# Kernel tuning notes

Hardware: AMD Instinct MI355X
Metric: run time of the kernel (lower is better)

## Reference

```python
import jax, jax.numpy as jnp
import numpy as np

N_NODES = 100000
N_EDGES = 1600000
D = 128        # in_dim == hidden_dim (forced by x_j + xe in message)
C = 64         # num_classes
G = 128        # number of graphs in the batch
BN_EPS = 1e-5


def setup_inputs() -> dict:
    key = jax.random.key(0)
    ks = jax.random.split(key, 14)
    s = 0.05
    inp = {
        "x": jax.random.normal(ks[0], (N_NODES, D), dtype=jnp.float32),
        "xe": jax.random.normal(ks[1], (N_EDGES, D), dtype=jnp.float32),
        "edge_index": jax.random.randint(ks[2], (2, N_EDGES), 0, N_NODES, dtype=jnp.int32),
        "batch": jnp.sort(jax.random.randint(ks[3], (N_NODES,), 0, G, dtype=jnp.int32)),
        # layer 0 MySAGEConv params
        "Wl0": jax.random.normal(ks[4], (D, D), dtype=jnp.float32) * s,
        "bl0": jnp.zeros((D,), dtype=jnp.float32),
        "Wr0": jax.random.normal(ks[5], (D, D), dtype=jnp.float32) * s,
        # layer 1 MySAGEConv params
        "Wl1": jax.random.normal(ks[6], (D, D), dtype=jnp.float32) * s,
        "bl1": jnp.zeros((D,), dtype=jnp.float32),
        "Wr1": jax.random.normal(ks[7], (D, D), dtype=jnp.float32) * s,
        # BatchNorm (only applied after non-final layers -> layer 0)
        "gamma0": jnp.ones((D,), dtype=jnp.float32),
        "beta0": jnp.zeros((D,), dtype=jnp.float32),
        # readout projection
        "Wp": jax.random.normal(ks[8], (C, D), dtype=jnp.float32) * s,
        "bp": jnp.zeros((C,), dtype=jnp.float32),
    }
    return inp


def _segment_mean(vals, idx, num_segments):
    s = jax.ops.segment_sum(vals, idx, num_segments=num_segments)
    cnt = jax.ops.segment_sum(jnp.ones((vals.shape[0],), vals.dtype), idx,
                              num_segments=num_segments)
    return s / jnp.clip(cnt, 1.0)[:, None]


def _my_sage_conv(h, xe, src, dst, Wl, bl, Wr):
    # message: relu(x_j + xe); aggregate: scatter-mean at dst; then lin_l + lin_r
    msg = jax.nn.relu(h[src] + xe)                       # [E, D]
    agg = _segment_mean(msg, dst, N_NODES)               # [N, D]
    return agg @ Wl.T + bl + h @ Wr.T


def _batchnorm_train(h, gamma, beta):
    mu = jnp.mean(h, axis=0)
    var = jnp.var(h, axis=0)
    return gamma * (h - mu) * jax.lax.rsqrt(var + BN_EPS) + beta


def reference(x, xe, edge_index, batch,
              Wl0, bl0, Wr0, Wl1, bl1, Wr1,
              gamma0, beta0, Wp, bp):
    src, dst = edge_index[0], edge_index[1]
    # layer 0: conv -> BN -> ReLU
    h = _my_sage_conv(x, xe, src, dst, Wl0, bl0, Wr0)
    h = jax.nn.relu(_batchnorm_train(h, gamma0, beta0))
    # layer 1 (last): conv only
    h = _my_sage_conv(h, xe, src, dst, Wl1, bl1, Wr1)
    # graph readout (global mean pool over pre-proj node features)
    g = _segment_mean(h, batch, G)                       # [G, D]
    # readout projection on nodes
    h = jax.nn.relu(h) @ Wp.T + bp                       # [N, C]
    return h, g
```

## Files before the change

### kernel.cpp

```cpp
#include <hip/hip_runtime.h>

#define N_NODES 100000
#define N_EDGES 1600000
#define DIM 128
#define NCLS 64
#define NG 128
#define BN_EPS 1e-5f

typedef __attribute__((ext_vector_type(8))) short s16x8;
typedef __attribute__((ext_vector_type(4))) float f32x4;
#define MFMA_BF16 __builtin_amdgcn_mfma_f32_16x16x32_bf16

__device__ __forceinline__ unsigned short f2b(float x) {
    unsigned u = __float_as_uint(x);
    return (unsigned short)((u + 0x7FFFu + ((u >> 16) & 1u)) >> 16);
}
__device__ __forceinline__ float b2f(unsigned short s) {
    return __uint_as_float(((unsigned)s) << 16);
}
__device__ __forceinline__ float4 bexp4(ushort4 u) {
    float4 f;
    f.x = b2f(u.x); f.y = b2f(u.y); f.z = b2f(u.z); f.w = b2f(u.w);
    return f;
}

__device__ __forceinline__ void f2hl8(float4 v0, float4 v1, s16x8& h8, s16x8& l8) {
    float vv[8] = {v0.x, v0.y, v0.z, v0.w, v1.x, v1.y, v1.z, v1.w};
#pragma unroll
    for (int i = 0; i < 8; ++i) {
        unsigned u = __float_as_uint(vv[i]);
        short h = (short)(u >> 16);
        float r = vv[i] - __uint_as_float(u & 0xFFFF0000u);
        short l = (short)(__float_as_uint(r) >> 16);
        h8[i] = h;
        l8[i] = l;
    }
}

__global__ __launch_bounds__(256) void k_mega0(
        const float* __restrict__ Wl0, const float* __restrict__ Wr0,
        const float* __restrict__ Wl1, const float* __restrict__ Wr1,
        const float* __restrict__ Wp,
        short* __restrict__ fWl0h, short* __restrict__ fWl0l,
        short* __restrict__ fWr0h, short* __restrict__ fWr0l,
        short* __restrict__ fWl1h, short* __restrict__ fWl1l,
        short* __restrict__ fWr1h, short* __restrict__ fWr1l,
        short* __restrict__ fWph, short* __restrict__ fWpl,
        const float* __restrict__ x, unsigned short* __restrict__ x_bf,
        const int* __restrict__ dst, int* __restrict__ cnt) {
    int b = blockIdx.x;
    if (b < 36) {
        const float* W; short* hi; short* lo; int ct;
        if (b < 8)       { W = Wl0; hi = fWl0h; lo = fWl0l; ct = b; }
        else if (b < 16) { W = Wr0; hi = fWr0h; lo = fWr0l; ct = b - 8; }
        else if (b < 24) { W = Wl1; hi = fWl1h; lo = fWl1l; ct = b - 16; }
        else if (b < 32) { W = Wr1; hi = fWr1h; lo = fWr1l; ct = b - 24; }
        else             { W = Wp;  hi = fWph;  lo = fWpl;  ct = b - 32; }
        if (b >= 32 && ct >= 4) return;
        int tt = threadIdx.x;
        int lane = tt & 63, ks = (tt >> 6) & 3;
        int row = ct * 16 + (lane & 15);
        int k0 = ks * 32 + ((lane >> 4) << 3);
        float4 v0 = *reinterpret_cast<const float4*>(&W[(size_t)row * DIM + k0]);
        float4 v1 = *reinterpret_cast<const float4*>(&W[(size_t)row * DIM + k0 + 4]);
        s16x8 h8, l8;
        f2hl8(v0, v1, h8, l8);
        int t = ct * 256 + ks * 64 + lane;
        *reinterpret_cast<s16x8*>(&hi[(size_t)t * 8]) = h8;
        *reinterpret_cast<s16x8*>(&lo[(size_t)t * 8]) = l8;
    } else if (b < 36 + 6250) {
        int i = (b - 36) * 256 + threadIdx.x;
        float4 a = reinterpret_cast<const float4*>(x)[(size_t)i * 2];
        float4 c = reinterpret_cast<const float4*>(x)[(size_t)i * 2 + 1];
        ushort4 oa, ob;
        oa.x = f2b(a.x); oa.y = f2b(a.y); oa.z = f2b(a.z); oa.w = f2b(a.w);
        ob.x = f2b(c.x); ob.y = f2b(c.y); ob.z = f2b(c.z); ob.w = f2b(c.w);
        reinterpret_cast<ushort4*>(x_bf)[(size_t)i * 2] = oa;
        reinterpret_cast<ushort4*>(x_bf)[(size_t)i * 2 + 1] = ob;
    } else {
        int e = (b - 36 - 6250) * 256 + threadIdx.x;
        atomicAdd(&cnt[dst[e]], 1);
    }
}

__global__ void k_scan1(const int* __restrict__ cnt, int* __restrict__ rowptr,
                        int* __restrict__ bsums) {
    __shared__ int sd[1024];
    int tid = threadIdx.x;
    int i = blockIdx.x * 1024 + tid;
    int v = (i < N_NODES) ? cnt[i] : 0;
    sd[tid] = v;
    __syncthreads();
    for (int off = 1; off < 1024; off <<= 1) {
        int t2 = (tid >= off) ? sd[tid - off] : 0;
        __syncthreads();
        sd[tid] += t2;
        __syncthreads();
    }
    if (i < N_NODES) rowptr[i] = sd[tid] - v;
    if (tid == 1023) bsums[blockIdx.x] = sd[tid];
}

__global__ void k_scan2(int* __restrict__ bsums, int nb) {
    __shared__ int sd[128];
    int t = threadIdx.x;
    int v = (t < nb) ? bsums[t] : 0;
    sd[t] = v;
    __syncthreads();
    for (int off = 1; off < 128; off <<= 1) {
        int u = (t >= off) ? sd[t - off] : 0;
        __syncthreads();
        sd[t] += u;
        __syncthreads();
    }
    if (t < nb) bsums[t] = sd[t] - v;
}

__global__ void k_scan3(int* __restrict__ rowptr, const int* __restrict__ bsums,
                        int* __restrict__ wcur) {
    int i = blockIdx.x * 1024 + threadIdx.x;
    if (i < N_NODES) {
        int v = rowptr[i] + bsums[blockIdx.x];
        rowptr[i] = v;
        wcur[i] = v;
    }
    if (i == N_NODES - 1) rowptr[N_NODES] = N_EDGES;
}

__global__ void k_scatter(const int* __restrict__ src, const int* __restrict__ dst,
                          int* __restrict__ wcur, int2* __restrict__ esort) {
    int e = blockIdx.x * 256 + threadIdx.x;
    if (e < N_EDGES) {
        int d = dst[e];
        int p = atomicAdd(&wcur[d], 1);
        esort[p] = make_int2(e, src[e]);
    }
}

template <int MODE>
__global__ __launch_bounds__(256) void k_agg(
        const unsigned short* __restrict__ Fb, const float* __restrict__ xe,
        unsigned short* __restrict__ xe_s,
        const int* __restrict__ rowptr, const int2* __restrict__ esort,
        unsigned short* __restrict__ agg, const float* __restrict__ bnsc) {
    int wid = (blockIdx.x * 256 + threadIdx.x) >> 6;
    int lane = threadIdx.x & 63;
    if (wid >= N_NODES) return;
    int half = lane >> 5;
    int l = lane & 31;
    int p0 = rowptr[wid], p1 = rowptr[wid + 1];
    if (p0 == p1) {
        if (half == 0) {
            ushort4 z = make_ushort4(0, 0, 0, 0);
            *reinterpret_cast<ushort4*>(&agg[(size_t)wid * DIM + l * 4]) = z;
        }
        return;
    }
    float4 sc, sh;
    if (MODE != 0) {
        sc = *reinterpret_cast<const float4*>(&bnsc[l * 4]);
        sh = *reinterpret_cast<const float4*>(&bnsc[DIM + l * 4]);
    }
    float4 acc = make_float4(0.f, 0.f, 0.f, 0.f);
    for (int p = p0; p < p1; p += 8) {
#pragma unroll
        for (int j = 0; j < 4; ++j) {
            int q = p + j * 2 + half;
            int qc = min(q, p1 - 1);
            int2 es = esort[qc];
            float4 a = bexp4(*reinterpret_cast<const ushort4*>(
                &Fb[(size_t)es.y * DIM + l * 4]));
            float4 b;
            if (MODE == 1) {
                b = bexp4(*reinterpret_cast<const ushort4*>(
                    &xe_s[(size_t)qc * DIM + l * 4]));
            } else {
                b = *reinterpret_cast<const float4*>(
                    &xe[(size_t)es.x * DIM + l * 4]);
            }
            if (MODE != 0) {
                a.x = fmaxf(a.x * sc.x + sh.x, 0.f);
                a.y = fmaxf(a.y * sc.y + sh.y, 0.f);
                a.z = fmaxf(a.z * sc.z + sh.z, 0.f);
                a.w = fmaxf(a.w * sc.w + sh.w, 0.f);
            }
            if (q < p1) {
                if (MODE == 0) {
                    ushort4 o;
                    o.x = f2b(b.x); o.y = f2b(b.y);
                    o.z = f2b(b.z); o.w = f2b(b.w);
                    *reinterpret_cast<ushort4*>(&xe_s[(size_t)qc * DIM + l * 4]) = o;
                }
                acc.x += fmaxf(a.x + b.x, 0.f);
                acc.y += fmaxf(a.y + b.y, 0.f);
                acc.z += fmaxf(a.z + b.z, 0.f);
                acc.w += fmaxf(a.w + b.w, 0.f);
            }
        }
    }
    acc.x += __shfl_xor(acc.x, 32);
    acc.y += __shfl_xor(acc.y, 32);
    acc.z += __shfl_xor(acc.z, 32);
    acc.w += __shfl_xor(acc.w, 32);
    if (half == 0) {
        float s = 1.f / (float)(p1 - p0);
        ushort4 o;
        o.x = f2b(acc.x * s); o.y = f2b(acc.y * s);
        o.z = f2b(acc.z * s); o.w = f2b(acc.w * s);
        *reinterpret_cast<ushort4*>(&agg[(size_t)wid * DIM + l * 4]) = o;
    }
}

__global__ __launch_bounds__(256) void k_gemm2(
        const unsigned short* __restrict__ Abf, const unsigned short* __restrict__ Bbf,
        const short* __restrict__ fW1h, const short* __restrict__ fW1l,
        const short* __restrict__ fW2h, const short* __restrict__ fW2l,
        const float* __restrict__ bias, unsigned short* __restrict__ OUTb,
        float* __restrict__ bnacc, const float* __restrict__ bnsc,
        int doBN, int bnB) {
    int t = threadIdx.x, w = t >> 6, l = t & 63;
    int n0 = blockIdx.x * 128;
    int r = l & 15, kh = l >> 4;
    int row0 = n0 + w * 16 + r;
    int row1 = row0 + 64;
    int n_0 = min(row0, N_NODES - 1);
    int n_1 = min(row1, N_NODES - 1);

    f32x4 acc0[8], acc1[8];
#pragma unroll
    for (int ct = 0; ct < 8; ++ct) {
        acc0[ct] = (f32x4){0.f, 0.f, 0.f, 0.f};
        acc1[ct] = (f32x4){0.f, 0.f, 0.f, 0.f};
    }
    const s16x8* w1h = (const s16x8*)fW1h;
    const s16x8* w1l = (const s16x8*)fW1l;
    const s16x8* w2h = (const s16x8*)fW2h;
    const s16x8* w2l = (const s16x8*)fW2l;

#pragma unroll
    for (int ks = 0; ks < 4; ++ks) {
        int kb = ks * 32 + kh * 8;
        s16x8 a0 = *reinterpret_cast<const s16x8*>(&Abf[(size_t)n_0 * DIM + kb]);
        s16x8 a1 = *reinterpret_cast<const s16x8*>(&Abf[(size_t)n_1 * DIM + kb]);
        s16x8 b0 = *reinterpret_cast<const s16x8*>(&Bbf[(size_t)n_0 * DIM + kb]);
        s16x8 b1 = *reinterpret_cast<const s16x8*>(&Bbf[(size_t)n_1 * DIM + kb]);
        if (bnB) {
            float4 sc0 = *reinterpret_cast<const float4*>(&bnsc[kb]);
            float4 sh0 = *reinterpret_cast<const float4*>(&bnsc[DIM + kb]);
            float4 sc1 = *reinterpret_cast<const float4*>(&bnsc[kb + 4]);
            float4 sh1 = *reinterpret_cast<const float4*>(&bnsc[DIM + kb + 4]);
            float scv[8] = {sc0.x, sc0.y, sc0.z, sc0.w, sc1.x, sc1.y, sc1.z, sc1.w};
            float shv[8] = {sh0.x, sh0.y, sh0.z, sh0.w, sh1.x, sh1.y, sh1.z, sh1.w};
#pragma unroll
            for (int i = 0; i < 8; ++i) {
                float v = b2f((unsigned short)b0[i]);
                b0[i] = (short)f2b(fmaxf(v * scv[i] + shv[i], 0.f));
                v = b2f((unsigned short)b1[i]);
                b1[i] = (short)f2b(fmaxf(v * scv[i] + shv[i], 0.f));
            }
        }
        int fb = ks * 64 + l;
#pragma unroll
        for (int ct = 0; ct < 8; ++ct) {
            int fi = ct * 256 + fb;
            s16x8 wh1 = w1h[fi], wl1 = w1l[fi];
            s16x8 wh2 = w2h[fi], wl2 = w2l[fi];
            acc0[ct] = MFMA_BF16(a0, wh1, acc0[ct], 0, 0, 0);
            acc0[ct] = MFMA_BF16(a0, wl1, acc0[ct], 0, 0, 0);
            acc0[ct] = MFMA_BF16(b0, wh2, acc0[ct], 0, 0, 0);
            acc0[ct] = MFMA_BF16(b0, wl2, acc0[ct], 0, 0, 0);
            acc1[ct] = MFMA_BF16(a1, wh1, acc1[ct], 0, 0, 0);
            acc1[ct] = MFMA_BF16(a1, wl1, acc1[ct], 0, 0, 0);
            acc1[ct] = MFMA_BF16(b1, wh2, acc1[ct], 0, 0, 0);
            acc1[ct] = MFMA_BF16(b1, wl2, acc1[ct], 0, 0, 0);
        }
    }

    float p1s[8], p2s[8];
    int col0 = l & 15;
    int nb0 = n0 + w * 16 + (kh << 2);
    int nb1 = nb0 + 64;
#pragma unroll
    for (int ct = 0; ct < 8; ++ct) {
        float bj = bias[ct * 16 + col0];
        float s1 = 0.f, s2 = 0.f;
#pragma unroll
        for (int rr = 0; rr < 4; ++rr) {
            int n = nb0 + rr;
            float h = acc0[ct][rr] + bj;
            if (n < N_NODES) {
                OUTb[(size_t)n * DIM + ct * 16 + col0] = f2b(h);
                s1 += h; s2 += h * h;
            }
            n = nb1 + rr;
            h = acc1[ct][rr] + bj;
            if (n < N_NODES) {
                OUTb[(size_t)n * DIM + ct * 16 + col0] = f2b(h);
                s1 += h; s2 += h * h;
            }
        }
        p1s[ct] = s1; p2s[ct] = s2;
    }
    if (doBN) {
        __shared__ float red1[512];
        __shared__ float red2[512];
#pragma unroll
        for (int ct = 0; ct < 8; ++ct) {
            p1s[ct] += __shfl_xor(p1s[ct], 16);
            p1s[ct] += __shfl_xor(p1s[ct], 32);
            p2s[ct] += __shfl_xor(p2s[ct], 16);
            p2s[ct] += __shfl_xor(p2s[ct], 32);
        }
        if (l < 16) {
#pragma unroll
            for (int ct = 0; ct < 8; ++ct) {
                red1[w * 128 + ct * 16 + l] = p1s[ct];
                red2[w * 128 + ct * 16 + l] = p2s[ct];
            }
        }
        __syncthreads();
        if (t < 128) {
            float s1 = red1[t] + red1[128 + t] + red1[256 + t] + red1[384 + t];
            float s2 = red2[t] + red2[128 + t] + red2[256 + t] + red2[384 + t];
            atomicAdd(&bnacc[t], s1);
            atomicAdd(&bnacc[128 + t], s2);
        }
    }
}

__global__ void k_bnfinal(const float* __restrict__ bnacc, const float* __restrict__ gamma,
                          const float* __restrict__ beta, float* __restrict__ bnsc) {
    int d = threadIdx.x;
    if (d < DIM) {
        float mu = bnacc[d] / (float)N_NODES;
        float var = bnacc[128 + d] / (float)N_NODES - mu * mu;
        float rstd = rsqrtf(var + BN_EPS);
        float sc = gamma[d] * rstd;
        bnsc[d] = sc;
        bnsc[128 + d] = beta[d] - mu * sc;
    }
}

__global__ void k_pool(const unsigned short* __restrict__ H1b,
                       const int* __restrict__ batch, float* __restrict__ gout) {
    __shared__ float red[4][128];
    int g = blockIdx.x;
    int t = threadIdx.x;
    int d = t & 127;
    int sl = t >> 7;
    int lo = 0, hi = N_NODES;
    while (lo < hi) { int m = (lo + hi) >> 1; if (batch[m] < g) lo = m + 1; else hi = m; }
    int s = lo;
    lo = 0; hi = N_NODES;
    while (lo < hi) { int m = (lo + hi) >> 1; if (batch[m] < g + 1) lo = m + 1; else hi = m; }
    int e = lo;
    float sum = 0.f;
    for (int n = s + sl; n < e; n += 4) sum += b2f(H1b[(size_t)n * DIM + d]);
    red[sl][d] = sum;
    __syncthreads();
    if (t < 128) {
        float tot = red[0][d] + red[1][d] + red[2][d] + red[3][d];
        gout[g * DIM + d] = tot / (float)max(e - s, 1);
    }
}

__global__ __launch_bounds__(256) void k_proj(
        const unsigned short* __restrict__ H1b, const short* __restrict__ fWph,
        const short* __restrict__ fWpl, const float* __restrict__ bp,
        float* __restrict__ OUT) {
    int t = threadIdx.x, w = t >> 6, l = t & 63;
    int n0 = blockIdx.x * 128;
    int r = l & 15, kh = l >> 4;
    int row0 = n0 + w * 16 + r;
    int row1 = row0 + 64;
    int n_0 = min(row0, N_NODES - 1);
    int n_1 = min(row1, N_NODES - 1);
    f32x4 acc0[4], acc1[4];
#pragma unroll
    for (int ct = 0; ct < 4; ++ct) {
        acc0[ct] = (f32x4){0.f, 0.f, 0.f, 0.f};
        acc1[ct] = (f32x4){0.f, 0.f, 0.f, 0.f};
    }
    const s16x8* wph = (const s16x8*)fWph;
    const s16x8* wpl = (const s16x8*)fWpl;
#pragma unroll
    for (int ks = 0; ks < 4; ++ks) {
        int kb = ks * 32 + kh * 8;
        s16x8 r0 = *reinterpret_cast<const s16x8*>(&H1b[(size_t)n_0 * DIM + kb]);
        s16x8 r1 = *reinterpret_cast<const s16x8*>(&H1b[(size_t)n_1 * DIM + kb]);
        s16x8 a0, a1;
#pragma unroll
        for (int i = 0; i < 8; ++i) {
            a0[i] = r0[i] < 0 ? (short)0 : r0[i];
            a1[i] = r1[i] < 0 ? (short)0 : r1[i];
        }
        int fb = ks * 64 + l;
#pragma unroll
        for (int ct = 0; ct < 4; ++ct) {
            int fi = ct * 256 + fb;
            s16x8 wh = wph[fi], wl = wpl[fi];
            acc0[ct] = MFMA_BF16(a0, wh, acc0[ct], 0, 0, 0);
            acc0[ct] = MFMA_BF16(a0, wl, acc0[ct], 0, 0, 0);
            acc1[ct] = MFMA_BF16(a1, wh, acc1[ct], 0, 0, 0);
            acc1[ct] = MFMA_BF16(a1, wl, acc1[ct], 0, 0, 0);
        }
    }
    int col0 = l & 15;
    int nb0 = n0 + w * 16 + (kh << 2);
    int nb1 = nb0 + 64;
#pragma unroll
    for (int ct = 0; ct < 4; ++ct) {
        float bj = bp[ct * 16 + col0];
#pragma unroll
        for (int rr = 0; rr < 4; ++rr) {
            int n = nb0 + rr;
            if (n < N_NODES)
                OUT[(size_t)n * NCLS + ct * 16 + col0] = acc0[ct][rr] + bj;
            n = nb1 + rr;
            if (n < N_NODES)
                OUT[(size_t)n * NCLS + ct * 16 + col0] = acc1[ct][rr] + bj;
        }
    }
}

extern "C" void kernel_launch(void* const* d_in, const int* in_sizes, int n_in,
                              void* d_out, int out_size, void* d_ws, size_t ws_size,
                              hipStream_t stream) {
    (void)in_sizes; (void)n_in; (void)out_size;
    const float* x     = (const float*)d_in[0];
    const float* xe    = (const float*)d_in[1];
    const int*   eidx  = (const int*)d_in[2];
    const int*   batch = (const int*)d_in[3];
    const float* Wl0   = (const float*)d_in[4];
    const float* bl0   = (const float*)d_in[5];
    const float* Wr0   = (const float*)d_in[6];
    const float* Wl1   = (const float*)d_in[7];
    const float* bl1   = (const float*)d_in[8];
    const float* Wr1   = (const float*)d_in[9];
    const float* gamma0 = (const float*)d_in[10];
    const float* beta0  = (const float*)d_in[11];
    const float* Wp    = (const float*)d_in[12];
    const float* bp    = (const float*)d_in[13];
    const int* srcp = eidx;
    const int* dstp = eidx + N_EDGES;

    char* ws = (char*)d_ws;
    size_t off = 0;
    auto carve = [&](size_t bytes) {
        void* p = ws + off;
        off = (off + bytes + 255) & ~(size_t)255;
        return p;
    };
    int*   cnt    = (int*)carve((size_t)N_NODES * 4);
    int*   rowptr = (int*)carve((size_t)(N_NODES + 1) * 4);
    int*   wcur   = (int*)carve((size_t)N_NODES * 4);
    int*   bsums  = (int*)carve(128 * 4);
    float* bnacc  = (float*)carve(256 * 4);
    float* bnsc   = (float*)carve(256 * 4);
    int2*  esort  = (int2*)carve((size_t)N_EDGES * 8);
    unsigned short* AGGb = (unsigned short*)carve((size_t)N_NODES * DIM * 2);
    unsigned short* x_bf = (unsigned short*)carve((size_t)N_NODES * DIM * 2);
    unsigned short* H_bf = (unsigned short*)carve((size_t)N_NODES * DIM * 2);
    unsigned short* H1b  = (unsigned short*)carve((size_t)N_NODES * DIM * 2);
    short* fWl0h = (short*)carve(16384 * 2);
    short* fWl0l = (short*)carve(16384 * 2);
    short* fWr0h = (short*)carve(16384 * 2);
    short* fWr0l = (short*)carve(16384 * 2);
    short* fWl1h = (short*)carve(16384 * 2);
    short* fWl1l = (short*)carve(16384 * 2);
    short* fWr1h = (short*)carve(16384 * 2);
    short* fWr1l = (short*)carve(16384 * 2);
    short* fWph  = (short*)carve(8192 * 2);
    short* fWpl  = (short*)carve(8192 * 2);

    size_t xes_bytes = (size_t)N_EDGES * DIM * 2;
    int seq = (off + xes_bytes + 256 <= ws_size) ? 1 : 0;
    unsigned short* xe_s = seq ? (unsigned short*)carve(xes_bytes) : nullptr;

    float* out_h = (float*)d_out;
    float* out_g = out_h + (size_t)N_NODES * NCLS;

    hipMemsetAsync(cnt, 0, (size_t)N_NODES * 4, stream);
    hipMemsetAsync(bnacc, 0, 256 * 4, stream);

    k_mega0<<<36 + 6250 + 6250, 256, 0, stream>>>(
        Wl0, Wr0, Wl1, Wr1, Wp,
        fWl0h, fWl0l, fWr0h, fWr0l, fWl1h, fWl1l, fWr1h, fWr1l, fWph, fWpl,
        x, x_bf, dstp, cnt);

    int nb = (N_NODES + 1023) / 1024;
    k_scan1<<<nb, 1024, 0, stream>>>(cnt, rowptr, bsums);
    k_scan2<<<1, 128, 0, stream>>>(bsums, nb);
    k_scan3<<<nb, 1024, 0, stream>>>(rowptr, bsums, wcur);
    k_scatter<<<(N_EDGES + 255) / 256, 256, 0, stream>>>(srcp, dstp, wcur, esort);

    int ablocks = (N_NODES * 64 + 255) / 256;
    int gblocks = (N_NODES + 127) / 128;

    if (seq)
        k_agg<0><<<ablocks, 256, 0, stream>>>(x_bf, xe, xe_s, rowptr, esort, AGGb, bnsc);
    else
        k_agg<2><<<ablocks, 256, 0, stream>>>(x_bf, xe, nullptr, rowptr, esort, AGGb, bnsc);
    k_gemm2<<<gblocks, 256, 0, stream>>>(AGGb, x_bf, fWl0h, fWl0l, fWr0h, fWr0l,
                                         bl0, H_bf, bnacc, bnsc, 1, 0);
    k_bnfinal<<<1, 128, 0, stream>>>(bnacc, gamma0, beta0, bnsc);

    if (seq)
        k_agg<1><<<ablocks, 256, 0, stream>>>(H_bf, xe, xe_s, rowptr, esort, AGGb, bnsc);
    else
        k_agg<2><<<ablocks, 256, 0, stream>>>(H_bf, xe, nullptr, rowptr, esort, AGGb, bnsc);
    k_gemm2<<<gblocks, 256, 0, stream>>>(AGGb, H_bf, fWl1h, fWl1l, fWr1h, fWr1l,
                                         bl1, H1b, bnacc, bnsc, 0, 1);

    k_pool<<<NG, 512, 0, stream>>>(H1b, batch, out_g);
    k_proj<<<gblocks, 256, 0, stream>>>(H1b, fWph, fWpl, bp, out_h);
}
```

Baseline: 862.5 us.

## Merge preprocessing into cooperative kernel, inline BN finalize, fuse pool with proj

Replaces the memsets, conversion/count kernel, three scan kernels and the scatter kernel with one cooperative grid-synchronised kernel of 512 blocks. The BN scale/shift is now recomputed from the accumulated sums inside the aggregation and GEMM kernels, so the separate BN-finalize launch goes away. The pooling and projection kernels become one launch. The aim is to cut launch overhead and inter-kernel gaps. In exchange, the grid-wide syncs cost something, the fixed 512-block grid may under-use the GPU in the atomic phases, and some BN work is recomputed per block.

Result: slower. 1.204 ms (+39.6%).

```diff
diff --git a/kernel.cpp b/kernel.cpp
--- a/kernel.cpp
+++ b/kernel.cpp
@@ -1,4 +1,7 @@
 #include <hip/hip_runtime.h>
+#include <hip/hip_cooperative_groups.h>
+
+namespace cg = cooperative_groups;
 
 #define N_NODES 100000
 #define N_EDGES 1600000
@@ -6,6 +9,8 @@
 #define NCLS 64
 #define NG 128
 #define BN_EPS 1e-5f
+#define COOP_BLOCKS 512
+#define GSZ (COOP_BLOCKS * 256)
 
 typedef __attribute__((ext_vector_type(8))) short s16x8;
 typedef __attribute__((ext_vector_type(4))) float f32x4;
@@ -37,7 +42,7 @@
     }
 }
 
-__global__ __launch_bounds__(256) void k_mega0(
+__global__ __launch_bounds__(256, 4) void k_coop(
         const float* __restrict__ Wl0, const float* __restrict__ Wr0,
         const float* __restrict__ Wl1, const float* __restrict__ Wr1,
         const float* __restrict__ Wp,
@@ -47,17 +52,29 @@
         short* __restrict__ fWr1h, short* __restrict__ fWr1l,
         short* __restrict__ fWph, short* __restrict__ fWpl,
         const float* __restrict__ x, unsigned short* __restrict__ x_bf,
-        const int* __restrict__ dst, int* __restrict__ cnt) {
-    int b = blockIdx.x;
-    if (b < 36) {
-        const float* W; short* hi; short* lo; int ct;
-        if (b < 8)       { W = Wl0; hi = fWl0h; lo = fWl0l; ct = b; }
-        else if (b < 16) { W = Wr0; hi = fWr0h; lo = fWr0l; ct = b - 8; }
-        else if (b < 24) { W = Wl1; hi = fWl1h; lo = fWl1l; ct = b - 16; }
-        else if (b < 32) { W = Wr1; hi = fWr1h; lo = fWr1l; ct = b - 24; }
-        else             { W = Wp;  hi = fWph;  lo = fWpl;  ct = b - 32; }
-        if (b >= 32 && ct >= 4) return;
-        int tt = threadIdx.x;
+        const int* __restrict__ src, const int* __restrict__ dst,
+        int* __restrict__ cnt, int* __restrict__ rowptr,
+        int* __restrict__ wcur, int* __restrict__ bsums,
+        float* __restrict__ bnacc, int2* __restrict__ esort) {
+    cg::grid_group grid = cg::this_grid();
+    __shared__ int sd[256];
+    int t = threadIdx.x;
+    int gtid = blockIdx.x * 256 + t;
+
+    for (int i = gtid; i < N_NODES; i += GSZ) cnt[i] = 0;
+    if (gtid < 256) bnacc[gtid] = 0.f;
+    for (int j = gtid; j < 9216; j += GSZ) {
+        const float* W; short* hi; short* lo; int ct, tt;
+        if (j < 8192) {
+            int m = j >> 11;
+            W  = (m == 0) ? Wl0 : (m == 1) ? Wr0 : (m == 2) ? Wl1 : Wr1;
+            hi = (m == 0) ? fWl0h : (m == 1) ? fWr0h : (m == 2) ? fWl1h : fWr1h;
+            lo = (m == 0) ? fWl0l : (m == 1) ? fWr0l : (m == 2) ? fWl1l : fWr1l;
+            ct = (j >> 8) & 7; tt = j & 255;
+        } else {
+            W = Wp; hi = fWph; lo = fWpl;
+            ct = (j - 8192) >> 8; tt = (j - 8192) & 255;
+        }
         int lane = tt & 63, ks = (tt >> 6) & 3;
         int row = ct * 16 + (lane & 15);
         int k0 = ks * 32 + ((lane >> 4) << 3);
@@ -65,11 +82,11 @@
         float4 v1 = *reinterpret_cast<const float4*>(&W[(size_t)row * DIM + k0 + 4]);
         s16x8 h8, l8;
         f2hl8(v0, v1, h8, l8);
-        int t = ct * 256 + ks * 64 + lane;
-        *reinterpret_cast<s16x8*>(&hi[(size_t)t * 8]) = h8;
-        *reinterpret_cast<s16x8*>(&lo[(size_t)t * 8]) = l8;
-    } else if (b < 36 + 6250) {
-        int i = (b - 36) * 256 + threadIdx.x;
+        int fi = ct * 256 + ks * 64 + lane;
+        *reinterpret_cast<s16x8*>(&hi[(size_t)fi * 8]) = h8;
+        *reinterpret_cast<s16x8*>(&lo[(size_t)fi * 8]) = l8;
+    }
+    for (int i = gtid; i < N_NODES * DIM / 8; i += GSZ) {
         float4 a = reinterpret_cast<const float4*>(x)[(size_t)i * 2];
         float4 c = reinterpret_cast<const float4*>(x)[(size_t)i * 2 + 1];
         ushort4 oa, ob;
@@ -77,60 +94,63 @@
         ob.x = f2b(c.x); ob.y = f2b(c.y); ob.z = f2b(c.z); ob.w = f2b(c.w);
         reinterpret_cast<ushort4*>(x_bf)[(size_t)i * 2] = oa;
         reinterpret_cast<ushort4*>(x_bf)[(size_t)i * 2 + 1] = ob;
-    } else {
-        int e = (b - 36 - 6250) * 256 + threadIdx.x;
-        atomicAdd(&cnt[dst[e]], 1);
-    }
-}
-
-__global__ void k_scan1(const int* __restrict__ cnt, int* __restrict__ rowptr,
-                        int* __restrict__ bsums) {
-    __shared__ int sd[1024];
-    int tid = threadIdx.x;
-    int i = blockIdx.x * 1024 + tid;
-    int v = (i < N_NODES) ? cnt[i] : 0;
-    sd[tid] = v;
-    __syncthreads();
-    for (int off = 1; off < 1024; off <<= 1) {
-        int t2 = (tid >= off) ? sd[tid - off] : 0;
+    }
+    grid.sync();
+
+    for (int e = gtid; e < N_EDGES; e += GSZ) atomicAdd(&cnt[dst[e]], 1);
+    grid.sync();
+
+    if (blockIdx.x < 98) {
+        int base = blockIdx.x * 1024;
+        int v[4]; int tsum = 0;
+#pragma unroll
+        for (int i = 0; i < 4; ++i) {
+            int idx = base + t * 4 + i;
+            v[i] = (idx < N_NODES) ? cnt[idx] : 0;
+            tsum += v[i];
+        }
+        sd[t] = tsum;
         __syncthreads();
-        sd[tid] += t2;
+        for (int off2 = 1; off2 < 256; off2 <<= 1) {
+            int u = (t >= off2) ? sd[t - off2] : 0;
+            __syncthreads();
+            sd[t] += u;
+            __syncthreads();
+        }
+        int run = sd[t] - tsum;
+#pragma unroll
+        for (int i = 0; i < 4; ++i) {
+            int idx = base + t * 4 + i;
+            if (idx < N_NODES) rowptr[idx] = run;
+            run += v[i];
+        }
+        if (t == 255) bsums[blockIdx.x] = sd[255];
+    }
+    grid.sync();
+
+    if (blockIdx.x == 0) {
+        int v = (t < 98) ? bsums[t] : 0;
+        sd[t] = v;
         __syncthreads();
-    }
-    if (i < N_NODES) rowptr[i] = sd[tid] - v;
-    if (tid == 1023) bsums[blockIdx.x] = sd[tid];
-}
-
-__global__ void k_scan2(int* __restrict__ bsums, int nb) {
-    __shared__ int sd[128];
-    int t = threadIdx.x;
-    int v = (t < nb) ? bsums[t] : 0;
-    sd[t] = v;
-    __syncthreads();
-    for (int off = 1; off < 128; off <<= 1) {
-        int u = (t >= off) ? sd[t - off] : 0;
-        __syncthreads();
-        sd[t] += u;
-        __syncthreads();
-    }
-    if (t < nb) bsums[t] = sd[t] - v;
-}
-
-__global__ void k_scan3(int* __restrict__ rowptr, const int* __restrict__ bsums,
-                        int* __restrict__ wcur) {
-    int i = blockIdx.x * 1024 + threadIdx.x;
-    if (i < N_NODES) {
-        int v = rowptr[i] + bsums[blockIdx.x];
-        rowptr[i] = v;
-        wcur[i] = v;
-    }
-    if (i == N_NODES - 1) rowptr[N_NODES] = N_EDGES;
-}
-
-__global__ void k_scatter(const int* __restrict__ src, const int* __restrict__ dst,
-                          int* __restrict__ wcur, int2* __restrict__ esort) {
-    int e = blockIdx.x * 256 + threadIdx.x;
-    if (e < N_EDGES) {
+        for (int off2 = 1; off2 < 256; off2 <<= 1) {
+            int u = (t >= off2) ? sd[t - off2] : 0;
+            __syncthreads();
+            sd[t] += u;
+            __syncthreads();
+        }
+        if (t < 98) bsums[t] = sd[t] - v;
+    }
+    grid.sync();
+
+    for (int i = gtid; i < N_NODES; i += GSZ) {
+        int val = rowptr[i] + bsums[i >> 10];
+        rowptr[i] = val;
+        wcur[i] = val;
+    }
+    if (gtid == 0) rowptr[N_NODES] = N_EDGES;
+    grid.sync();
+
+    for (int e = gtid; e < N_EDGES; e += GSZ) {
         int d = dst[e];
         int p = atomicAdd(&wcur[d], 1);
         esort[p] = make_int2(e, src[e]);
@@ -142,7 +162,8 @@
         const unsigned short* __restrict__ Fb, const float* __restrict__ xe,
         unsigned short* __restrict__ xe_s,
         const int* __restrict__ rowptr, const int2* __restrict__ esort,
-        unsigned short* __restrict__ agg, const float* __restrict__ bnsc) {
+        unsigned short* __restrict__ agg, const float* __restrict__ bnacc,
+        const float* __restrict__ gamma, const float* __restrict__ beta) {
     int wid = (blockIdx.x * 256 + threadIdx.x) >> 6;
     int lane = threadIdx.x & 63;
     if (wid >= N_NODES) return;
@@ -156,10 +177,17 @@
         }
         return;
     }
-    float4 sc, sh;
+    float scv[4], shv[4];
     if (MODE != 0) {
-        sc = *reinterpret_cast<const float4*>(&bnsc[l * 4]);
-        sh = *reinterpret_cast<const float4*>(&bnsc[DIM + l * 4]);
+#pragma unroll
+        for (int i = 0; i < 4; ++i) {
+            int d = l * 4 + i;
+            float mu = bnacc[d] * (1.f / N_NODES);
+            float var = bnacc[128 + d] * (1.f / N_NODES) - mu * mu;
+            float rstd = rsqrtf(var + BN_EPS);
+            scv[i] = gamma[d] * rstd;
+            shv[i] = beta[d] - mu * scv[i];
+        }
     }
     float4 acc = make_float4(0.f, 0.f, 0.f, 0.f);
     for (int p = p0; p < p1; p += 8) {
@@ -179,10 +207,10 @@
                     &xe[(size_t)es.x * DIM + l * 4]);
             }
             if (MODE != 0) {
-                a.x = fmaxf(a.x * sc.x + sh.x, 0.f);
-                a.y = fmaxf(a.y * sc.y + sh.y, 0.f);
-                a.z = fmaxf(a.z * sc.z + sh.z, 0.f);
-                a.w = fmaxf(a.w * sc.w + sh.w, 0.f);
+                a.x = fmaxf(a.x * scv[0] + shv[0], 0.f);
+                a.y = fmaxf(a.y * scv[1] + shv[1], 0.f);
+                a.z = fmaxf(a.z * scv[2] + shv[2], 0.f);
+                a.w = fmaxf(a.w * scv[3] + shv[3], 0.f);
             }
             if (q < p1) {
                 if (MODE == 0) {
@@ -216,9 +244,21 @@
         const short* __restrict__ fW1h, const short* __restrict__ fW1l,
         const short* __restrict__ fW2h, const short* __restrict__ fW2l,
         const float* __restrict__ bias, unsigned short* __restrict__ OUTb,
-        float* __restrict__ bnacc, const float* __restrict__ bnsc,
-        int doBN, int bnB) {
+        float* __restrict__ bnacc, const float* __restrict__ gamma,
+        const float* __restrict__ beta, int doBN, int bnB) {
+    __shared__ float bnsc_s[256];
     int t = threadIdx.x, w = t >> 6, l = t & 63;
+    if (bnB) {
+        if (t < 128) {
+            float mu = bnacc[t] * (1.f / N_NODES);
+            float var = bnacc[128 + t] * (1.f / N_NODES) - mu * mu;
+            float rstd = rsqrtf(var + BN_EPS);
+            float sc = gamma[t] * rstd;
+            bnsc_s[t] = sc;
+            bnsc_s[128 + t] = beta[t] - mu * sc;
+        }
+        __syncthreads();
+    }
     int n0 = blockIdx.x * 128;
     int r = l & 15, kh = l >> 4;
     int row0 = n0 + w * 16 + r;
@@ -245,18 +285,13 @@
         s16x8 b0 = *reinterpret_cast<const s16x8*>(&Bbf[(size_t)n_0 * DIM + kb]);
         s16x8 b1 = *reinterpret_cast<const s16x8*>(&Bbf[(size_t)n_1 * DIM + kb]);
         if (bnB) {
-            float4 sc0 = *reinterpret_cast<const float4*>(&bnsc[kb]);
-            float4 sh0 = *reinterpret_cast<const float4*>(&bnsc[DIM + kb]);
-            float4 sc1 = *reinterpret_cast<const float4*>(&bnsc[kb + 4]);
-            float4 sh1 = *reinterpret_cast<const float4*>(&bnsc[DIM + kb + 4]);
-            float scv[8] = {sc0.x, sc0.y, sc0.z, sc0.w, sc1.x, sc1.y, sc1.z, sc1.w};
-            float shv[8] = {sh0.x, sh0.y, sh0.z, sh0.w, sh1.x, sh1.y, sh1.z, sh1.w};
 #pragma unroll
             for (int i = 0; i < 8; ++i) {
+                int d = kb + i;
                 float v = b2f((unsigned short)b0[i]);
-                b0[i] = (short)f2b(fmaxf(v * scv[i] + shv[i], 0.f));
+                b0[i] = (short)f2b(fmaxf(v * bnsc_s[d] + bnsc_s[128 + d], 0.f));
                 v = b2f((unsigned short)b1[i]);
-                b1[i] = (short)f2b(fmaxf(v * scv[i] + shv[i], 0.f));
+                b1[i] = (short)f2b(fmaxf(v * bnsc_s[d] + bnsc_s[128 + d], 0.f));
             }
         }
         int fb = ks * 64 + l;
@@ -328,48 +363,33 @@
     }
 }
 
-__global__ void k_bnfinal(const float* __restrict__ bnacc, const float* __restrict__ gamma,
-                          const float* __restrict__ beta, float* __restrict__ bnsc) {
-    int d = threadIdx.x;
-    if (d < DIM) {
-        float mu = bnacc[d] / (float)N_NODES;
-        float var = bnacc[128 + d] / (float)N_NODES - mu * mu;
-        float rstd = rsqrtf(var + BN_EPS);
-        float sc = gamma[d] * rstd;
-        bnsc[d] = sc;
-        bnsc[128 + d] = beta[d] - mu * sc;
-    }
-}
-
-__global__ void k_pool(const unsigned short* __restrict__ H1b,
-                       const int* __restrict__ batch, float* __restrict__ gout) {
-    __shared__ float red[4][128];
-    int g = blockIdx.x;
-    int t = threadIdx.x;
-    int d = t & 127;
-    int sl = t >> 7;
-    int lo = 0, hi = N_NODES;
-    while (lo < hi) { int m = (lo + hi) >> 1; if (batch[m] < g) lo = m + 1; else hi = m; }
-    int s = lo;
-    lo = 0; hi = N_NODES;
-    while (lo < hi) { int m = (lo + hi) >> 1; if (batch[m] < g + 1) lo = m + 1; else hi = m; }
-    int e = lo;
-    float sum = 0.f;
-    for (int n = s + sl; n < e; n += 4) sum += b2f(H1b[(size_t)n * DIM + d]);
-    red[sl][d] = sum;
-    __syncthreads();
-    if (t < 128) {
-        float tot = red[0][d] + red[1][d] + red[2][d] + red[3][d];
-        gout[g * DIM + d] = tot / (float)max(e - s, 1);
-    }
-}
-
-__global__ __launch_bounds__(256) void k_proj(
-        const unsigned short* __restrict__ H1b, const short* __restrict__ fWph,
+__global__ __launch_bounds__(256) void k_poolproj(
+        const unsigned short* __restrict__ H1b, const int* __restrict__ batch,
+        float* __restrict__ gout, const short* __restrict__ fWph,
         const short* __restrict__ fWpl, const float* __restrict__ bp,
         float* __restrict__ OUT) {
-    int t = threadIdx.x, w = t >> 6, l = t & 63;
-    int n0 = blockIdx.x * 128;
+    int t = threadIdx.x;
+    if (blockIdx.x < NG) {
+        __shared__ float red[2][128];
+        int g = blockIdx.x;
+        int d = t & 127;
+        int sl = t >> 7;
+        int lo = 0, hi = N_NODES;
+        while (lo < hi) { int m = (lo + hi) >> 1; if (batch[m] < g) lo = m + 1; else hi = m; }
+        int s = lo;
+        lo = 0; hi = N_NODES;
+        while (lo < hi) { int m = (lo + hi) >> 1; if (batch[m] < g + 1) lo = m + 1; else hi = m; }
+        int e = lo;
+        float sum = 0.f;
+        for (int n = s + sl; n < e; n += 2) sum += b2f(H1b[(size_t)n * DIM + d]);
+        red[sl][d] = sum;
+        __syncthreads();
+        if (t < 128)
+            gout[g * DIM + d] = (red[0][d] + red[1][d]) / (float)max(e - s, 1);
+        return;
+    }
+    int w = t >> 6, l = t & 63;
+    int n0 = (blockIdx.x - NG) * 128;
     int r = l & 15, kh = l >> 4;
     int row0 = n0 + w * 16 + r;
     int row1 = row0 + 64;
@@ -456,7 +476,6 @@
     int*   wcur   = (int*)carve((size_t)N_NODES * 4);
     int*   bsums  = (int*)carve(128 * 4);
     float* bnacc  = (float*)carve(256 * 4);
-    float* bnsc   = (float*)carve(256 * 4);
     int2*  esort  = (int2*)carve((size_t)N_EDGES * 8);
     unsigned short* AGGb = (unsigned short*)carve((size_t)N_NODES * DIM * 2);
     unsigned short* x_bf = (unsigned short*)carve((size_t)N_NODES * DIM * 2);
@@ -480,38 +499,39 @@
     float* out_h = (float*)d_out;
     float* out_g = out_h + (size_t)N_NODES * NCLS;
 
-    hipMemsetAsync(cnt, 0, (size_t)N_NODES * 4, stream);
-    hipMemsetAsync(bnacc, 0, 256 * 4, stream);
-
-    k_mega0<<<36 + 6250 + 6250, 256, 0, stream>>>(
-        Wl0, Wr0, Wl1, Wr1, Wp,
-        fWl0h, fWl0l, fWr0h, fWr0l, fWl1h, fWl1l, fWr1h, fWr1l, fWph, fWpl,
-        x, x_bf, dstp, cnt);
-
-    int nb = (N_NODES + 1023) / 1024;
-    k_scan1<<<nb, 1024, 0, stream>>>(cnt, rowptr, bsums);
-    k_scan2<<<1, 128, 0, stream>>>(bsums, nb);
-    k_scan3<<<nb, 1024, 0, stream>>>(rowptr, bsums, wcur);
-    k_scatter<<<(N_EDGES + 255) / 256, 256, 0, stream>>>(srcp, dstp, wcur, esort);
+    void* args[] = {
+        (void*)&Wl0, (void*)&Wr0, (void*)&Wl1, (void*)&Wr1, (void*)&Wp,
+        (void*)&fWl0h, (void*)&fWl0l, (void*)&fWr0h, (void*)&fWr0l,
+        (void*)&fWl1h, (void*)&fWl1l, (void*)&fWr1h, (void*)&fWr1l,
+        (void*)&fWph, (void*)&fWpl,
+        (void*)&x, (void*)&x_bf, (void*)&srcp, (void*)&dstp,
+        (void*)&cnt, (void*)&rowptr, (void*)&wcur, (void*)&bsums,
+        (void*)&bnacc, (void*)&esort
+    };
+    hipLaunchCooperativeKernel((const void*)k_coop, dim3(COOP_BLOCKS), dim3(256),
+                               args, 0, stream);
 
     int ablocks = (N_NODES * 64 + 255) / 256;
     int gblocks = (N_NODES + 127) / 128;
 
     if (seq)
-        k_agg<0><<<ablocks, 256, 0, stream>>>(x_bf, xe, xe_s, rowptr, esort, AGGb, bnsc);
+        k_agg<0><<<ablocks, 256, 0, stream>>>(x_bf, xe, xe_s, rowptr, esort, AGGb,
+                                              nullptr, nullptr, nullptr);
     else
-        k_agg<2><<<ablocks, 256, 0, stream>>>(x_bf, xe, nullptr, rowptr, esort, AGGb, bnsc);
+        k_agg<2><<<ablocks, 256, 0, stream>>>(x_bf, xe, nullptr, rowptr, esort, AGGb,
+                                              bnacc, gamma0, beta0);
     k_gemm2<<<gblocks, 256, 0, stream>>>(AGGb, x_bf, fWl0h, fWl0l, fWr0h, fWr0l,
-                                         bl0, H_bf, bnacc, bnsc, 1, 0);
-    k_bnfinal<<<1, 128, 0, stream>>>(bnacc, gamma0, beta0, bnsc);
+                                         bl0, H_bf, bnacc, gamma0, beta0, 1, 0);
 
     if (seq)
-        k_agg<1><<<ablocks, 256, 0, stream>>>(H_bf, xe, xe_s, rowptr, esort, AGGb, bnsc);
+        k_agg<1><<<ablocks, 256, 0, stream>>>(H_bf, xe, xe_s, rowptr, esort, AGGb,
+                                              bnacc, gamma0, beta0);
     else
-        k_agg<2><<<ablocks, 256, 0, stream>>>(H_bf, xe, nullptr, rowptr, esort, AGGb, bnsc);
+        k_agg<2><<<ablocks, 256, 0, stream>>>(H_bf, xe, nullptr, rowptr, esort, AGGb,
+                                              bnacc, gamma0, beta0);
     k_gemm2<<<gblocks, 256, 0, stream>>>(AGGb, H_bf, fWl1h, fWl1l, fWr1h, fWr1l,
-                                         bl1, H1b, bnacc, bnsc, 0, 1);
-
-    k_pool<<<NG, 512, 0, stream>>>(H1b, batch, out_g);
-    k_proj<<<gblocks, 256, 0, stream>>>(H1b, fWph, fWpl, bp, out_h);
-}
+                                         bl1, H1b, bnacc, gamma0, beta0, 0, 1);
+
+    k_poolproj<<<NG + gblocks, 256, 0, stream>>>(H1b, batch, out_g,
+                                                 fWph, fWpl, bp, out_h);
+}
```

## Fold BN finalize into consumers, prefetch edge indices via shuffles, fuse pool+proj

Applied to the files above, without the earlier changes.

Removes the separate BN-finalize kernel and the bnacc memset by zeroing bnacc in the first kernel and recomputing scale and shift inside each consumer kernel. In the aggregation kernel, the sorted edge entries for the next group of 8 are prefetched into lanes and broadcast with shuffles, instead of every lane loading its own esort entry. The pooling and projection kernels are merged into one launch. The goal is fewer launches and less index-load latency, at the cost of redundant BN math in every block and an extra barrier in the GEMM.

Result: no change. 853.8 us (-1.0%).

```diff
diff --git a/kernel.cpp b/kernel.cpp
--- a/kernel.cpp
+++ b/kernel.cpp
@@ -47,8 +47,10 @@
         short* __restrict__ fWr1h, short* __restrict__ fWr1l,
         short* __restrict__ fWph, short* __restrict__ fWpl,
         const float* __restrict__ x, unsigned short* __restrict__ x_bf,
-        const int* __restrict__ dst, int* __restrict__ cnt) {
+        const int* __restrict__ dst, int* __restrict__ cnt,
+        float* __restrict__ bnacc) {
     int b = blockIdx.x;
+    if (b == 0) bnacc[threadIdx.x] = 0.f;
     if (b < 36) {
         const float* W; short* hi; short* lo; int ct;
         if (b < 8)       { W = Wl0; hi = fWl0h; lo = fWl0l; ct = b; }
@@ -142,7 +144,8 @@
         const unsigned short* __restrict__ Fb, const float* __restrict__ xe,
         unsigned short* __restrict__ xe_s,
         const int* __restrict__ rowptr, const int2* __restrict__ esort,
-        unsigned short* __restrict__ agg, const float* __restrict__ bnsc) {
+        unsigned short* __restrict__ agg, const float* __restrict__ bnacc,
+        const float* __restrict__ gamma, const float* __restrict__ beta) {
     int wid = (blockIdx.x * 256 + threadIdx.x) >> 6;
     int lane = threadIdx.x & 63;
     if (wid >= N_NODES) return;
@@ -156,40 +159,53 @@
         }
         return;
     }
-    float4 sc, sh;
+    float scv[4], shv[4];
     if (MODE != 0) {
-        sc = *reinterpret_cast<const float4*>(&bnsc[l * 4]);
-        sh = *reinterpret_cast<const float4*>(&bnsc[DIM + l * 4]);
+#pragma unroll
+        for (int i = 0; i < 4; ++i) {
+            int d = l * 4 + i;
+            float mu = bnacc[d] * (1.f / N_NODES);
+            float var = bnacc[128 + d] * (1.f / N_NODES) - mu * mu;
+            float rstd = rsqrtf(var + BN_EPS);
+            scv[i] = gamma[d] * rstd;
+            shv[i] = beta[d] - mu * scv[i];
+        }
     }
     float4 acc = make_float4(0.f, 0.f, 0.f, 0.f);
+    int2 ev = esort[min(p0 + (lane & 7), p1 - 1)];
     for (int p = p0; p < p1; p += 8) {
+        int pn = p + 8;
+        int2 evn;
+        if (pn < p1) evn = esort[min(pn + (lane & 7), p1 - 1)];
 #pragma unroll
         for (int j = 0; j < 4; ++j) {
-            int q = p + j * 2 + half;
-            int qc = min(q, p1 - 1);
-            int2 es = esort[qc];
+            int k = j * 2 + half;
+            int q = p + k;
+            int esx = __shfl(ev.x, k);
+            int esy = __shfl(ev.y, k);
             float4 a = bexp4(*reinterpret_cast<const ushort4*>(
-                &Fb[(size_t)es.y * DIM + l * 4]));
+                &Fb[(size_t)esy * DIM + l * 4]));
             float4 b;
             if (MODE == 1) {
+                int qc = min(q, p1 - 1);
                 b = bexp4(*reinterpret_cast<const ushort4*>(
                     &xe_s[(size_t)qc * DIM + l * 4]));
             } else {
                 b = *reinterpret_cast<const float4*>(
-                    &xe[(size_t)es.x * DIM + l * 4]);
+                    &xe[(size_t)esx * DIM + l * 4]);
             }
             if (MODE != 0) {
-                a.x = fmaxf(a.x * sc.x + sh.x, 0.f);
-                a.y = fmaxf(a.y * sc.y + sh.y, 0.f);
-                a.z = fmaxf(a.z * sc.z + sh.z, 0.f);
-                a.w = fmaxf(a.w * sc.w + sh.w, 0.f);
+                a.x = fmaxf(a.x * scv[0] + shv[0], 0.f);
+                a.y = fmaxf(a.y * scv[1] + shv[1], 0.f);
+                a.z = fmaxf(a.z * scv[2] + shv[2], 0.f);
+                a.w = fmaxf(a.w * scv[3] + shv[3], 0.f);
             }
             if (q < p1) {
                 if (MODE == 0) {
                     ushort4 o;
                     o.x = f2b(b.x); o.y = f2b(b.y);
                     o.z = f2b(b.z); o.w = f2b(b.w);
-                    *reinterpret_cast<ushort4*>(&xe_s[(size_t)qc * DIM + l * 4]) = o;
+                    *reinterpret_cast<ushort4*>(&xe_s[(size_t)q * DIM + l * 4]) = o;
                 }
                 acc.x += fmaxf(a.x + b.x, 0.f);
                 acc.y += fmaxf(a.y + b.y, 0.f);
@@ -197,6 +213,7 @@
                 acc.w += fmaxf(a.w + b.w, 0.f);
             }
         }
+        if (pn < p1) ev = evn;
     }
     acc.x += __shfl_xor(acc.x, 32);
     acc.y += __shfl_xor(acc.y, 32);
@@ -216,9 +233,21 @@
         const short* __restrict__ fW1h, const short* __restrict__ fW1l,
         const short* __restrict__ fW2h, const short* __restrict__ fW2l,
         const float* __restrict__ bias, unsigned short* __restrict__ OUTb,
-        float* __restrict__ bnacc, const float* __restrict__ bnsc,
-        int doBN, int bnB) {
+        float* __restrict__ bnacc, const float* __restrict__ gamma,
+        const float* __restrict__ beta, int doBN, int bnB) {
+    __shared__ float bnsc_s[256];
     int t = threadIdx.x, w = t >> 6, l = t & 63;
+    if (bnB) {
+        if (t < 128) {
+            float mu = bnacc[t] * (1.f / N_NODES);
+            float var = bnacc[128 + t] * (1.f / N_NODES) - mu * mu;
+            float rstd = rsqrtf(var + BN_EPS);
+            float sc = gamma[t] * rstd;
+            bnsc_s[t] = sc;
+            bnsc_s[128 + t] = beta[t] - mu * sc;
+        }
+        __syncthreads();
+    }
     int n0 = blockIdx.x * 128;
     int r = l & 15, kh = l >> 4;
     int row0 = n0 + w * 16 + r;
@@ -245,18 +274,13 @@
         s16x8 b0 = *reinterpret_cast<const s16x8*>(&Bbf[(size_t)n_0 * DIM + kb]);
         s16x8 b1 = *reinterpret_cast<const s16x8*>(&Bbf[(size_t)n_1 * DIM + kb]);
         if (bnB) {
-            float4 sc0 = *reinterpret_cast<const float4*>(&bnsc[kb]);
-            float4 sh0 = *reinterpret_cast<const float4*>(&bnsc[DIM + kb]);
-            float4 sc1 = *reinterpret_cast<const float4*>(&bnsc[kb + 4]);
-            float4 sh1 = *reinterpret_cast<const float4*>(&bnsc[DIM + kb + 4]);
-            float scv[8] = {sc0.x, sc0.y, sc0.z, sc0.w, sc1.x, sc1.y, sc1.z, sc1.w};
-            float shv[8] = {sh0.x, sh0.y, sh0.z, sh0.w, sh1.x, sh1.y, sh1.z, sh1.w};
 #pragma unroll
             for (int i = 0; i < 8; ++i) {
+                int d = kb + i;
                 float v = b2f((unsigned short)b0[i]);
-                b0[i] = (short)f2b(fmaxf(v * scv[i] + shv[i], 0.f));
+                b0[i] = (short)f2b(fmaxf(v * bnsc_s[d] + bnsc_s[128 + d], 0.f));
                 v = b2f((unsigned short)b1[i]);
-                b1[i] = (short)f2b(fmaxf(v * scv[i] + shv[i], 0.f));
+                b1[i] = (short)f2b(fmaxf(v * bnsc_s[d] + bnsc_s[128 + d], 0.f));
             }
         }
         int fb = ks * 64 + l;
@@ -328,48 +352,33 @@
     }
 }
 
-__global__ void k_bnfinal(const float* __restrict__ bnacc, const float* __restrict__ gamma,
-                          const float* __restrict__ beta, float* __restrict__ bnsc) {
-    int d = threadIdx.x;
-    if (d < DIM) {
-        float mu = bnacc[d] / (float)N_NODES;
-        float var = bnacc[128 + d] / (float)N_NODES - mu * mu;
-        float rstd = rsqrtf(var + BN_EPS);
-        float sc = gamma[d] * rstd;
-        bnsc[d] = sc;
-        bnsc[128 + d] = beta[d] - mu * sc;
-    }
-}
-
-__global__ void k_pool(const unsigned short* __restrict__ H1b,
-                       const int* __restrict__ batch, float* __restrict__ gout) {
-    __shared__ float red[4][128];
-    int g = blockIdx.x;
-    int t = threadIdx.x;
-    int d = t & 127;
-    int sl = t >> 7;
-    int lo = 0, hi = N_NODES;
-    while (lo < hi) { int m = (lo + hi) >> 1; if (batch[m] < g) lo = m + 1; else hi = m; }
-    int s = lo;
-    lo = 0; hi = N_NODES;
-    while (lo < hi) { int m = (lo + hi) >> 1; if (batch[m] < g + 1) lo = m + 1; else hi = m; }
-    int e = lo;
-    float sum = 0.f;
-    for (int n = s + sl; n < e; n += 4) sum += b2f(H1b[(size_t)n * DIM + d]);
-    red[sl][d] = sum;
-    __syncthreads();
-    if (t < 128) {
-        float tot = red[0][d] + red[1][d] + red[2][d] + red[3][d];
-        gout[g * DIM + d] = tot / (float)max(e - s, 1);
-    }
-}
-
-__global__ __launch_bounds__(256) void k_proj(
-        const unsigned short* __restrict__ H1b, const short* __restrict__ fWph,
+__global__ __launch_bounds__(256) void k_poolproj(
+        const unsigned short* __restrict__ H1b, const int* __restrict__ batch,
+        float* __restrict__ gout, const short* __restrict__ fWph,
         const short* __restrict__ fWpl, const float* __restrict__ bp,
         float* __restrict__ OUT) {
-    int t = threadIdx.x, w = t >> 6, l = t & 63;
-    int n0 = blockIdx.x * 128;
+    int t = threadIdx.x;
+    if (blockIdx.x < NG) {
+        __shared__ float red[2][128];
+        int g = blockIdx.x;
+        int d = t & 127;
+        int sl = t >> 7;
+        int lo = 0, hi = N_NODES;
+        while (lo < hi) { int m = (lo + hi) >> 1; if (batch[m] < g) lo = m + 1; else hi = m; }
+        int s = lo;
+        lo = 0; hi = N_NODES;
+        while (lo < hi) { int m = (lo + hi) >> 1; if (batch[m] < g + 1) lo = m + 1; else hi = m; }
+        int e = lo;
+        float sum = 0.f;
+        for (int n = s + sl; n < e; n += 2) sum += b2f(H1b[(size_t)n * DIM + d]);
+        red[sl][d] = sum;
+        __syncthreads();
+        if (t < 128)
+            gout[g * DIM + d] = (red[0][d] + red[1][d]) / (float)max(e - s, 1);
+        return;
+    }
+    int w = t >> 6, l = t & 63;
+    int n0 = (blockIdx.x - NG) * 128;
     int r = l & 15, kh = l >> 4;
     int row0 = n0 + w * 16 + r;
     int row1 = row0 + 64;
@@ -456,7 +465,6 @@
     int*   wcur   = (int*)carve((size_t)N_NODES * 4);
     int*   bsums  = (int*)carve(128 * 4);
     float* bnacc  = (float*)carve(256 * 4);
-    float* bnsc   = (float*)carve(256 * 4);
     int2*  esort  = (int2*)carve((size_t)N_EDGES * 8);
     unsigned short* AGGb = (unsigned short*)carve((size_t)N_NODES * DIM * 2);
     unsigned short* x_bf = (unsigned short*)carve((size_t)N_NODES * DIM * 2);
@@ -481,12 +489,11 @@
     float* out_g = out_h + (size_t)N_NODES * NCLS;
 
     hipMemsetAsync(cnt, 0, (size_t)N_NODES * 4, stream);
-    hipMemsetAsync(bnacc, 0, 256 * 4, stream);
 
     k_mega0<<<36 + 6250 + 6250, 256, 0, stream>>>(
         Wl0, Wr0, Wl1, Wr1, Wp,
         fWl0h, fWl0l, fWr0h, fWr0l, fWl1h, fWl1l, fWr1h, fWr1l, fWph, fWpl,
-        x, x_bf, dstp, cnt);
+        x, x_bf, dstp, cnt, bnacc);
 
     int nb = (N_NODES + 1023) / 1024;
     k_scan1<<<nb, 1024, 0, stream>>>(cnt, rowptr, bsums);
@@ -498,20 +505,23 @@
     int gblocks = (N_NODES + 127) / 128;
 
     if (seq)
-        k_agg<0><<<ablocks, 256, 0, stream>>>(x_bf, xe, xe_s, rowptr, esort, AGGb, bnsc);
+        k_agg<0><<<ablocks, 256, 0, stream>>>(x_bf, xe, xe_s, rowptr, esort, AGGb,
+                                              nullptr, nullptr, nullptr);
     else
-        k_agg<2><<<ablocks, 256, 0, stream>>>(x_bf, xe, nullptr, rowptr, esort, AGGb, bnsc);
+        k_agg<2><<<ablocks, 256, 0, stream>>>(x_bf, xe, nullptr, rowptr, esort, AGGb,
+                                              bnacc, gamma0, beta0);
     k_gemm2<<<gblocks, 256, 0, stream>>>(AGGb, x_bf, fWl0h, fWl0l, fWr0h, fWr0l,
-                                         bl0, H_bf, bnacc, bnsc, 1, 0);
-    k_bnfinal<<<1, 128, 0, stream>>>(bnacc, gamma0, beta0, bnsc);
+                                         bl0, H_bf, bnacc, gamma0, beta0, 1, 0);
 
     if (seq)
-        k_agg<1><<<ablocks, 256, 0, stream>>>(H_bf, xe, xe_s, rowptr, esort, AGGb, bnsc);
+        k_agg<1><<<ablocks, 256, 0, stream>>>(H_bf, xe, xe_s, rowptr, esort, AGGb,
+                                              bnacc, gamma0, beta0);
     else
-        k_agg<2><<<ablocks, 256, 0, stream>>>(H_bf, xe, nullptr, rowptr, esort, AGGb, bnsc);
+        k_agg<2><<<ablocks, 256, 0, stream>>>(H_bf, xe, nullptr, rowptr, esort, AGGb,
+                                              bnacc, gamma0, beta0);
     k_gemm2<<<gblocks, 256, 0, stream>>>(AGGb, H_bf, fWl1h, fWl1l, fWr1h, fWr1l,
-                                         bl1, H1b, bnacc, bnsc, 0, 1);
-
-    k_pool<<<NG, 512, 0, stream>>>(H1b, batch, out_g);
-    k_proj<<<gblocks, 256, 0, stream>>>(H1b, fWph, fWpl, bp, out_h);
-}
+                                         bl1, H1b, bnacc, gamma0, beta0, 0, 1);
+
+    k_poolproj<<<NG + gblocks, 256, 0, stream>>>(H1b, batch, out_g,
+                                                 fWph, fWpl, bp, out_h);
+}
```
